# Performance work log

Measured on AMD Instinct MI355X. Metric: run time of the kernel, lower is better.

## Reference

```python
import jax, jax.numpy as jnp
import numpy as np
import math

B, T = 32, 64
VOCAB = 50005
EMB = 512
HID = 1024
SES = 1024
KNOW = 8785
NEG = math.exp(-100)

def _glorot(key, shape):
    fan_in, fan_out = shape[1], shape[0]
    lim = (6.0 / (fan_in + fan_out)) ** 0.5
    return jax.random.uniform(key, shape, jnp.float32, -lim, lim)

def setup_inputs() -> dict:
    key = jax.random.key(0)
    ks = jax.random.split(key, 16)
    inp = {}
    inp['ses_encoding'] = jax.random.normal(ks[0], (B, 1, SES), jnp.float32)
    inp['know_encoding'] = jax.random.normal(ks[1], (B, 1, SES), jnp.float32)
    inp['target'] = jax.random.randint(ks[2], (B, T), 0, 50000)
    inp['embed_w'] = jax.random.normal(ks[3], (VOCAB, EMB), jnp.float32) * 0.02
    # GRU params (PyTorch layout: W_ih [3H, E], W_hh [3H, H], gate order r,z,n)
    s = 1.0 / (HID ** 0.5)
    inp['W_ih'] = jax.random.uniform(ks[4], (3 * HID, EMB), jnp.float32, -s, s)
    inp['W_hh'] = jax.random.uniform(ks[5], (3 * HID, HID), jnp.float32, -s, s)
    inp['b_ih'] = jax.random.uniform(ks[6], (3 * HID,), jnp.float32, -s, s)
    inp['b_hh'] = jax.random.uniform(ks[7], (3 * HID,), jnp.float32, -s, s)
    inp['ses_to_dec_w'] = _glorot(ks[8], (HID, SES))
    inp['ses_to_dec_b'] = jnp.zeros((HID,), jnp.float32)
    inp['dec_inf_w'] = _glorot(ks[9], (2 * EMB, HID))
    inp['ses_inf_w'] = _glorot(ks[10], (2 * EMB, SES))
    inp['emb_inf_w'] = _glorot(ks[11], (2 * EMB, EMB))
    inp['emb_inf_b'] = jnp.zeros((2 * EMB,), jnp.float32)
    inp['W1'] = jax.random.normal(ks[12], (VOCAB, SES), jnp.float32) * 0.02
    inp['W2'] = jax.random.normal(ks[13], (VOCAB, SES), jnp.float32) * 0.02
    inp['W3'] = jax.random.normal(ks[14], (VOCAB, 2 * EMB), jnp.float32) * 0.02
    inp['W4'] = jax.random.normal(ks[15], (VOCAB, EMB), jnp.float32) * 0.02
    inp['know_vote_w'] = _glorot(jax.random.fold_in(key, 99), (KNOW, SES))
    return inp

def _gru_step(x, h, W_ih, W_hh, b_ih, b_hh):
    # x: [B,E], h: [B,H]
    gi = x @ W_ih.T + b_ih
    gh = h @ W_hh.T + b_hh
    ir, iz, inn = jnp.split(gi, 3, axis=-1)
    hr, hz, hn = jnp.split(gh, 3, axis=-1)
    r = jax.nn.sigmoid(ir + hr)
    z = jax.nn.sigmoid(iz + hz)
    n = jnp.tanh(inn + r * hn)
    return (1.0 - z) * h + z * n  # torch: h' = (1-z)*n + z*h with torch z; note torch formula

def _gru_step_torch(x, h, W_ih, W_hh, b_ih, b_hh):
    gi = x @ W_ih.T + b_ih
    gh = h @ W_hh.T + b_hh
    ir, iz, inn = jnp.split(gi, 3, axis=-1)
    hr, hz, hn = jnp.split(gh, 3, axis=-1)
    r = jax.nn.sigmoid(ir + hr)
    z = jax.nn.sigmoid(iz + hz)
    n = jnp.tanh(inn + r * hn)
    return (1.0 - z) * n + z * h

def reference(ses_encoding, know_encoding, target, embed_w, W_ih, W_hh, b_ih, b_hh,
              ses_to_dec_w, ses_to_dec_b, dec_inf_w, ses_inf_w, emb_inf_w, emb_inf_b,
              W1, W2, W3, W4, know_vote_w):
    ses = ses_encoding[:, 0, :]    # [B, SES]
    know = know_encoding[:, 0, :]  # [B, SES]
    target_emb = embed_w[target]   # [B, T, E]

    h0 = jnp.tanh(ses @ ses_to_dec_w.T + ses_to_dec_b)  # [B, H]

    # time-invariant pieces
    ses_inf_vec = ses @ ses_inf_w.T                      # [B, 2E]
    l1 = ses @ W1.T                                      # [B, V]
    l2 = know @ W2.T                                     # [B, V]
    # knowledge mixture log-probs (constant over time)
    ks = know @ know_vote_w.T                            # [B, KNOW]
    ks = ks[:, :-1]                                      # drop last -> [B, KNOW-1]
    pad_l = jnp.full((ks.shape[0], 10), NEG, ks.dtype)
    pad_r = jnp.full((ks.shape[0], VOCAB - 10 - (KNOW - 1)), NEG, ks.dtype)
    know_scores = jnp.concatenate([pad_l, ks, pad_r], axis=1)  # [B, V]
    know_probs = jax.nn.log_softmax(know_scores, axis=-1)      # [B, V]
    gate_const = l1 + l2                                 # [B, V]

    def step(h, emb_t):
        # emb_t: [B, E]
        h_new = _gru_step_torch(emb_t, h, W_ih, W_hh, b_ih, b_hh)  # [B, H]
        dec_hid_vec = h_new @ dec_inf_w.T                          # [B, 2E]
        target_inf = emb_t @ emb_inf_w.T + emb_inf_b               # [B, 2E]
        total = dec_hid_vec + ses_inf_vec + target_inf             # [B, 2E]
        mx = jnp.max(total.reshape(total.shape[0], EMB, 2), axis=-1)  # maxout -> [B, E]
        logits = mx @ embed_w.T                                    # shared embedding -> [B, V]
        hid_probs = jax.nn.log_softmax(logits, axis=-1)
        l3 = h_new @ W3.T                                          # note: W3 applied to hid_o [B,H]... but W3 is [V,2E]
        l4 = emb_t @ W4.T                                          # [B, V]
        gate = jax.nn.sigmoid(gate_const + l3 + l4)                # [B, V]
        final = gate * hid_probs + (1.0 - gate) * know_probs       # [B, V]
        return h_new, final

    # target_emb time-major for scan
    _, outs = jax.lax.scan(step, h0, jnp.swapaxes(target_emb, 0, 1))
    final_scores_all = jnp.swapaxes(outs, 0, 1)  # [B, T, V]
    return final_scores_all
```

## Files before the change

### kernel.cpp

```cpp
#include <hip/hip_runtime.h>

constexpr int VOC  = 50005;
constexpr int VOCP = 50048;
constexpr int VOCP2= 50176;
constexpr int NTM  = 391;
constexpr int NTMP = 400;
constexpr int KSN  = 8784;
constexpr int KSNP = 8832;
constexpr float NPAD = 41221.0f;

typedef unsigned short u16;
typedef __attribute__((ext_vector_type(4))) float f32x4;
typedef __attribute__((ext_vector_type(8))) short bf16x8;

__device__ __forceinline__ float dot4(float4 a, float4 b) {
    return a.x*b.x + a.y*b.y + a.z*b.z + a.w*b.w;
}
__device__ __forceinline__ float sigmoidf_(float x) { return 1.0f / (1.0f + expf(-x)); }
__device__ __forceinline__ u16 f2bf(float f) {
    unsigned x = __float_as_uint(f);
    return (u16)((x + 0x7FFFu + ((x >> 16) & 1u)) >> 16);
}
__device__ __forceinline__ float bf2f(u16 u) { return __uint_as_float(((unsigned)u) << 16); }
template<int AUX>
__device__ __forceinline__ void gload_lds16x(const void* g, void* l) {
    __builtin_amdgcn_global_load_lds((const __attribute__((address_space(1))) unsigned int*)g,
                                     (__attribute__((address_space(3))) unsigned int*)l, 16, 0, AUX);
}
__device__ __forceinline__ void gload_lds16(const void* g, void* l) { gload_lds16x<0>(g, l); }
__device__ __forceinline__ void store_u16_sc(u16* p, u16 v) {
    asm volatile("global_store_short %0, %1, off sc0 sc1" :: "v"(p), "v"((unsigned)v) : "memory");
}

__global__ __launch_bounds__(256) void k_cvt(const float* __restrict__ src, u16* __restrict__ dst,
                                             int ncols, int sld, int dld) {
    int row = blockIdx.x;
    int c = (blockIdx.y * 256 + threadIdx.x) * 4;
    if (c >= ncols) return;
    float4 v = *(const float4*)(src + (size_t)row * sld + c);
    unsigned lo = f2bf(v.x) | ((unsigned)f2bf(v.y) << 16);
    unsigned hi = f2bf(v.z) | ((unsigned)f2bf(v.w) << 16);
    *(uint2*)(dst + (size_t)row * dld + c) = make_uint2(lo, hi);
}

__global__ __launch_bounds__(256) void k_pad0(u16* __restrict__ Aemb, u16* __restrict__ A34,
                                              u16* __restrict__ Awk) {
    int r = VOC + blockIdx.x;
    unsigned* p3 = (unsigned*)(A34 + (size_t)r * 1536);
    for (int i = threadIdx.x; i < 768; i += 256) p3[i] = 0;
    if (r < VOCP) {
        unsigned* pe = (unsigned*)(Aemb + (size_t)r * 512);
        if (threadIdx.x < 256) pe[threadIdx.x] = 0;
        unsigned* pw = (unsigned*)(Awk + (size_t)r * 2048);
        for (int i = threadIdx.x; i < 1024; i += 256) pw[i] = 0;
    }
}
__global__ __launch_bounds__(256) void k_padK(u16* __restrict__ kvwb) {
    int r = KSN + blockIdx.x;
    unsigned* p = (unsigned*)(kvwb + (size_t)r * 1024);
    for (int i = threadIdx.x; i < 512; i += 256) p[i] = 0;
}

__global__ __launch_bounds__(256) void k_bsk(const float* __restrict__ ses,
                                             const float* __restrict__ know,
                                             u16* __restrict__ Bsk) {
    int row = blockIdx.x;
    for (int c0 = threadIdx.x * 4; c0 < 2048; c0 += 1024) {
        uint2 val = make_uint2(0, 0);
        if (row < 32) {
            const float* srcp = (c0 < 1024) ? ses + (size_t)row * 1024 + c0
                                            : know + (size_t)row * 1024 + (c0 - 1024);
            float4 v = *(const float4*)srcp;
            val = make_uint2(f2bf(v.x) | ((unsigned)f2bf(v.y) << 16),
                             f2bf(v.z) | ((unsigned)f2bf(v.w) << 16));
        }
        *(uint2*)(Bsk + (size_t)row * 2048 + c0) = val;
    }
}

__global__ __launch_bounds__(128) void k_gather(const float* __restrict__ embed,
                                                const int* __restrict__ target,
                                                u16* __restrict__ BG) {
    int n = blockIdx.x;
    int row = target[n];
    int c = threadIdx.x * 4;
    float4 v = *(const float4*)(embed + (size_t)row * 512 + c);
    unsigned lo = f2bf(v.x) | ((unsigned)f2bf(v.y) << 16);
    unsigned hi = f2bf(v.z) | ((unsigned)f2bf(v.w) << 16);
    *(uint2*)(BG + (size_t)n * 1536 + 1024 + c) = make_uint2(lo, hi);
}

__global__ __launch_bounds__(256) void k_h0_sesinf(const float* __restrict__ ses,
                                                   const float* __restrict__ sdw,
                                                   const float* __restrict__ sdb,
                                                   const float* __restrict__ siw,
                                                   float* __restrict__ h0,
                                                   float* __restrict__ sesinf) {
    int g = blockIdx.x * 256 + threadIdx.x;
    int b = g & 31;
    int jg = g >> 5;
    int j0 = jg * 4;
    const float4* s4 = (const float4*)(ses + (size_t)b * 1024);
    const float4* wa[4];
    const float4* wc[4];
#pragma unroll
    for (int r = 0; r < 4; ++r) {
        wa[r] = (const float4*)(sdw + (size_t)(j0 + r) * 1024);
        wc[r] = (const float4*)(siw + (size_t)(j0 + r) * 1024);
    }
    float a[4] = {0, 0, 0, 0}, c[4] = {0, 0, 0, 0};
    for (int kq = 0; kq < 256; ++kq) {
        float4 sv = s4[kq];
#pragma unroll
        for (int r = 0; r < 4; ++r) { a[r] += dot4(sv, wa[r][kq]); c[r] += dot4(sv, wc[r][kq]); }
    }
#pragma unroll
    for (int r = 0; r < 4; ++r) {
        h0[b * 1024 + j0 + r] = tanhf(a[r] + sdb[j0 + r]);
        sesinf[b * 1024 + j0 + r] = c[r];
    }
}

__global__ __launch_bounds__(256) void k_lseknow(const float* __restrict__ ks,
                                                 float* __restrict__ lsek) {
    int b = blockIdx.x;
    int t = threadIdx.x;
    __shared__ float sm[256];
    float m = -1e30f;
    for (int j = t; j < KSN; j += 256) m = fmaxf(m, ks[(size_t)b * KSN + j]);
    sm[t] = m;
    __syncthreads();
    for (int s = 128; s > 0; s >>= 1) { if (t < s) sm[t] = fmaxf(sm[t], sm[t + s]); __syncthreads(); }
    m = fmaxf(sm[0], 0.0f);
    __syncthreads();
    float s = 0.0f;
    for (int j = t; j < KSN; j += 256) s += expf(ks[(size_t)b * KSN + j] - m);
    sm[t] = s;
    __syncthreads();
    for (int r = 128; r > 0; r >>= 1) { if (t < r) sm[t] += sm[t + r]; __syncthreads(); }
    if (t == 0) lsek[b] = m + logf(sm[0] + NPAD * expf(0.0f - m));
}

template<int EPI>
__global__ __launch_bounds__(256) void gemm_bt(
    const u16* __restrict__ A, int lda,
    const u16* __restrict__ B, int ldb, int K,
    const float* __restrict__ p0, const float* __restrict__ p1,
    float* __restrict__ q0, u16* __restrict__ q1,
    unsigned char* __restrict__ q2, float* __restrict__ q3)
{
    __shared__ u16 Asm[128 * 64];
    __shared__ u16 Bsm[128 * 64];
    const int tid = threadIdx.x;
    const int lane = tid & 63;
    const int w = tid >> 6;
    const int wm = w >> 1, wn = w & 1;
    const int nt = blockIdx.x, mt = blockIdx.y;

    f32x4 acc[4][4];
#pragma unroll
    for (int i = 0; i < 4; ++i)
#pragma unroll
        for (int j = 0; j < 4; ++j) acc[i][j] = (f32x4){0.f, 0.f, 0.f, 0.f};

    for (int kt = 0; kt < K; kt += 64) {
#pragma unroll
        for (int p = 0; p < 4; ++p) {
            int flat = (w * 4 + p) * 64 + lane;
            int row = flat >> 3, slot = flat & 7;
            int ss = slot ^ (row & 7);
            gload_lds16(A + (size_t)(mt * 128 + row) * lda + kt + ss * 8, Asm + flat * 8);
            gload_lds16(B + (size_t)(nt * 128 + row) * ldb + kt + ss * 8, Bsm + flat * 8);
        }
        __syncthreads();
#pragma unroll
        for (int kc = 0; kc < 2; ++kc) {
            bf16x8 af[4], bfr[4];
#pragma unroll
            for (int mi = 0; mi < 4; ++mi) {
                int row = wm * 64 + mi * 16 + (lane & 15);
                int bcol = kc * 64 + ((lane >> 4) << 4);
                af[mi] = *(const bf16x8*)((const char*)Asm + row * 128 + (bcol ^ ((row & 7) << 4)));
            }
#pragma unroll
            for (int ni = 0; ni < 4; ++ni) {
                int row = wn * 64 + ni * 16 + (lane & 15);
                int bcol = kc * 64 + ((lane >> 4) << 4);
                bfr[ni] = *(const bf16x8*)((const char*)Bsm + row * 128 + (bcol ^ ((row & 7) << 4)));
            }
#pragma unroll
            for (int mi = 0; mi < 4; ++mi)
#pragma unroll
                for (int ni = 0; ni < 4; ++ni)
                    acc[mi][ni] = __builtin_amdgcn_mfma_f32_16x16x32_bf16(af[mi], bfr[ni], acc[mi][ni], 0, 0, 0);
        }
        __syncthreads();
    }

    const int cl = lane & 15;
    const int rg = (lane >> 4) << 2;

    if constexpr (EPI == 0) {
#pragma unroll
        for (int mi = 0; mi < 4; ++mi) {
            int m0 = mt * 128 + wm * 64 + mi * 16 + rg;
            float4 bias = *(const float4*)(p0 + m0);
#pragma unroll
            for (int ni = 0; ni < 4; ++ni) {
                int n = nt * 128 + wn * 64 + ni * 16 + cl;
                float4 v;
                v.x = acc[mi][ni][0] + bias.x; v.y = acc[mi][ni][1] + bias.y;
                v.z = acc[mi][ni][2] + bias.z; v.w = acc[mi][ni][3] + bias.w;
                *(float4*)(q0 + (size_t)n * 3072 + m0) = v;
            }
        }
    }
    if constexpr (EPI == 1) {
#pragma unroll
        for (int mi = 0; mi < 4; ++mi) {
            int m0 = mt * 128 + wm * 64 + mi * 16 + rg;
            float4 eb4 = *(const float4*)(p1 + m0);
#pragma unroll
            for (int ni = 0; ni < 4; ++ni) {
                int n = nt * 128 + wn * 64 + ni * 16 + cl;
                int b = n >> 6;
                float v0 = acc[mi][ni][0] + p0[b * 1024 + m0 + 0] + eb4.x;
                float v1 = acc[mi][ni][1] + p0[b * 1024 + m0 + 1] + eb4.y;
                float v2 = acc[mi][ni][2] + p0[b * 1024 + m0 + 2] + eb4.z;
                float v3 = acc[mi][ni][3] + p0[b * 1024 + m0 + 3] + eb4.w;
                unsigned pk = f2bf(fmaxf(v0, v1)) | ((unsigned)f2bf(fmaxf(v2, v3)) << 16);
                *(unsigned*)(q1 + (size_t)n * 512 + (m0 >> 1)) = pk;
            }
        }
    }
    if constexpr (EPI == 3) {
        __shared__ float redm[2][128];
        __shared__ float reds[2][128];
#pragma unroll
        for (int mi = 0; mi < 4; ++mi) {
            int v0 = mt * 128 + wm * 64 + mi * 16 + rg;
#pragma unroll
            for (int ni = 0; ni < 4; ++ni) {
                int n = nt * 128 + wn * 64 + ni * 16 + cl;
                unsigned lo = f2bf(acc[mi][ni][0]) | ((unsigned)f2bf(acc[mi][ni][1]) << 16);
                unsigned hi = f2bf(acc[mi][ni][2]) | ((unsigned)f2bf(acc[mi][ni][3]) << 16);
                *(uint2*)(q1 + (size_t)n * VOCP + v0) = make_uint2(lo, hi);
            }
        }
#pragma unroll
        for (int ni = 0; ni < 4; ++ni) {
            float lm = -1e30f;
#pragma unroll
            for (int mi = 0; mi < 4; ++mi) {
                int v0 = mt * 128 + wm * 64 + mi * 16 + rg;
#pragma unroll
                for (int r = 0; r < 4; ++r)
                    if (v0 + r < VOC) lm = fmaxf(lm, acc[mi][ni][r]);
            }
            lm = fmaxf(lm, __shfl_xor(lm, 16));
            lm = fmaxf(lm, __shfl_xor(lm, 32));
            float s = 0.0f;
#pragma unroll
            for (int mi = 0; mi < 4; ++mi) {
                int v0 = mt * 128 + wm * 64 + mi * 16 + rg;
#pragma unroll
                for (int r = 0; r < 4; ++r)
                    if (v0 + r < VOC) s += expf(acc[mi][ni][r] - lm);
            }
            s += __shfl_xor(s, 16);
            s += __shfl_xor(s, 32);
            if (lane < 16) {
                redm[wm][wn * 64 + ni * 16 + lane] = lm;
                reds[wm][wn * 64 + ni * 16 + lane] = s;
            }
        }
        __syncthreads();
        if (tid < 128) {
            float m0_ = redm[0][tid], m1_ = redm[1][tid];
            float m = fmaxf(m0_, m1_);
            float s = reds[0][tid] * expf(m0_ - m) + reds[1][tid] * expf(m1_ - m);
            int n = nt * 128 + tid;
            q0[(size_t)n * NTMP + mt] = m;
            q3[(size_t)n * NTMP + mt] = s;
        }
    }
    if constexpr (EPI == 4) {
#pragma unroll
        for (int mi = 0; mi < 4; ++mi) {
            int m0 = mt * 128 + wm * 64 + mi * 16 + rg;
#pragma unroll
            for (int ni = 0; ni < 4; ++ni) {
                int n = nt * 128 + wn * 64 + ni * 16 + cl;
                if (n < 32) {
                    float4 v;
                    v.x = acc[mi][ni][0]; v.y = acc[mi][ni][1];
                    v.z = acc[mi][ni][2]; v.w = acc[mi][ni][3];
                    *(float4*)(q0 + (size_t)n * VOCP2 + m0) = v;
                }
            }
        }
    }
    if constexpr (EPI == 5) {
#pragma unroll
        for (int mi = 0; mi < 4; ++mi) {
            int m0 = mt * 128 + wm * 64 + mi * 16 + rg;
#pragma unroll
            for (int ni = 0; ni < 4; ++ni) {
                int n = nt * 128 + wn * 64 + ni * 16 + cl;
                if (n < 32 && m0 < KSN) {
                    float4 v;
                    v.x = acc[mi][ni][0]; v.y = acc[mi][ni][1];
                    v.z = acc[mi][ni][2]; v.w = acc[mi][ni][3];
                    *(float4*)(q0 + (size_t)n * KSN + m0) = v;
                }
            }
        }
    }
}

__global__ __launch_bounds__(512, 1) void gemm_gate8(
    const u16* __restrict__ A,
    const u16* __restrict__ B,
    const float* __restrict__ gc2,
    unsigned char* __restrict__ g8)
{
    __shared__ __align__(16) char smem[131072];
    const int tid = threadIdx.x;
    const int lane = tid & 63;
    const int w = tid >> 6;
    const int wm = w >> 2;
    const int wn = w & 3;
    const int lrow = lane & 15;
    const int g = lane >> 4;

    int bid = blockIdx.x;
    int wg = (bid & 7) * 196 + (bid >> 3);
    int mt = wg >> 3;
    int nt = wg & 7;
    const size_t arow0 = (size_t)mt * 256;
    const size_t brow0 = (size_t)nt * 256;

    auto stageA = [&](int T, int h) {
        char* dst = smem + (T & 1) * 65536 + h * 16384;
        const u16* src = A + (arow0 + h * 128) * 1536 + T * 64;
#pragma unroll
        for (int q = 0; q < 2; ++q) {
            int flat = q * 512 + tid;
            int r = flat >> 3, s = flat & 7;
            int ss = s ^ (r & 7);
            gload_lds16(src + (size_t)r * 1536 + ss * 8, dst + flat * 16);
        }
    };
    auto stageB = [&](int T, int h) {
        char* dst = smem + (T & 1) * 65536 + 32768 + h * 16384;
        const u16* src = B + (brow0 + h * 128) * 1536 + T * 64;
#pragma unroll
        for (int q = 0; q < 2; ++q) {
            int flat = q * 512 + tid;
            int r = flat >> 3, s = flat & 7;
            int ss = s ^ (r & 7);
            gload_lds16(src + (size_t)r * 1536 + ss * 8, dst + flat * 16);
        }
    };

    f32x4 acc[8][4];
#pragma unroll
    for (int i = 0; i < 8; ++i)
#pragma unroll
        for (int j = 0; j < 4; ++j) acc[i][j] = (f32x4){0.f, 0.f, 0.f, 0.f};

    bf16x8 bf[4][2];
    auto loadB_ = [&](int d) {
        char* Bb = smem + d * 65536 + 32768 + (wn >> 1) * 16384;
#pragma unroll
        for (int ni = 0; ni < 4; ++ni) {
            int r = (wn & 1) * 64 + ni * 16 + lrow;
#pragma unroll
            for (int kk = 0; kk < 2; ++kk)
                bf[ni][kk] = *(const bf16x8*)(Bb + r * 128 + ((kk * 64 + g * 16) ^ ((r & 7) << 4)));
        }
    };

#define GPH(D, Q, LB, STG, VM)                                                        \
    {                                                                                 \
        if (LB) loadB_(D);                                                            \
        bf16x8 af[2][2];                                                              \
        char* Ab = smem + (D) * 65536 + wm * 16384;                                   \
        _Pragma("unroll") for (int mi = 0; mi < 2; ++mi) {                            \
            int r = ((Q) * 2 + mi) * 16 + lrow;                                       \
            _Pragma("unroll") for (int kk = 0; kk < 2; ++kk)                          \
                af[mi][kk] = *(const bf16x8*)(Ab + r * 128 +                          \
                                ((kk * 64 + g * 16) ^ ((r & 7) << 4)));               \
        }                                                                             \
        STG;                                                                          \
        __builtin_amdgcn_s_barrier();                                                 \
        asm volatile("s_waitcnt lgkmcnt(0)" ::: "memory");                            \
        __builtin_amdgcn_sched_barrier(0);                                            \
        __builtin_amdgcn_s_setprio(1);                                                \
        _Pragma("unroll") for (int kk = 0; kk < 2; ++kk)                              \
            _Pragma("unroll") for (int mi = 0; mi < 2; ++mi)                          \
                _Pragma("unroll") for (int ni = 0; ni < 4; ++ni)                      \
                    acc[(Q) * 2 + mi][ni] = __builtin_amdgcn_mfma_f32_16x16x32_bf16(  \
                        af[mi][kk], bf[ni][kk], acc[(Q) * 2 + mi][ni], 0, 0, 0);      \
        __builtin_amdgcn_s_setprio(0);                                                \
        VM;                                                                           \
        __builtin_amdgcn_s_barrier();                                                 \
    }
#define VM4 asm volatile("s_waitcnt vmcnt(4)" ::: "memory"); __builtin_amdgcn_sched_barrier(0)
#define VM0 asm volatile("s_waitcnt vmcnt(0)" ::: "memory"); __builtin_amdgcn_sched_barrier(0)
#define NOP (void)0

    stageB(0, 0); stageB(0, 1); stageA(0, 0); stageA(0, 1); stageB(1, 0); stageB(1, 1);
    VM4;
    __builtin_amdgcn_s_barrier();

    for (int i = 0; i < 11; ++i) {
        int T0 = 2 * i, T1 = 2 * i + 1;
        GPH(0, 0, true,  stageA(T1, 0),     NOP);
        GPH(0, 1, false, stageA(T1, 1),     NOP);
        GPH(0, 2, false, stageB(T0 + 2, 0), NOP);
        GPH(0, 3, false, stageB(T0 + 2, 1), VM4);
        GPH(1, 0, true,  stageA(T0 + 2, 0), NOP);
        GPH(1, 1, false, stageA(T0 + 2, 1), NOP);
        GPH(1, 2, false, stageB(T1 + 2, 0), NOP);
        GPH(1, 3, false, stageB(T1 + 2, 1), VM4);
    }
    GPH(0, 0, true,  stageA(23, 0), NOP);
    GPH(0, 1, false, stageA(23, 1), NOP);
    GPH(0, 2, false, NOP,           NOP);
    GPH(0, 3, false, NOP,           VM0);
    GPH(1, 0, true,  NOP,           NOP);
    GPH(1, 1, false, NOP,           NOP);
    GPH(1, 2, false, NOP,           NOP);
    GPH(1, 3, false, NOP,           NOP);
#undef GPH
#undef VM4
#undef VM0
#undef NOP

    const int rg = g << 2;
    const int b = nt * 4 + wn;
    const float* gcrow = gc2 + (size_t)b * VOCP2;
#pragma unroll
    for (int m = 0; m < 8; ++m) {
        int v0 = mt * 256 + wm * 128 + m * 16 + rg;
        float4 gcv = *(const float4*)(gcrow + v0);
#pragma unroll
        for (int ni = 0; ni < 4; ++ni) {
            int n = nt * 256 + wn * 64 + ni * 16 + lrow;
            unsigned pk = 0;
#pragma unroll
            for (int r = 0; r < 4; ++r) {
                float garg = acc[m][ni][r] + ((const float*)&gcv)[r];
                float gate = 1.0f / (1.0f + expf(-garg));
                pk |= ((unsigned)(int)(gate * 255.0f + 0.5f)) << (8 * r);
            }
            *(unsigned*)(g8 + (size_t)n * VOCP2 + v0) = pk;
        }
    }
}

__global__ __launch_bounds__(256, 1) void k_gru_m4(const u16* __restrict__ WhhB,
                                                   const float* __restrict__ GI,
                                                   const float* __restrict__ bhh,
                                                   const u16* __restrict__ h0b,
                                                   u16* __restrict__ BG,
                                                   unsigned* __restrict__ flags) {
    __shared__ __align__(16) char smem[131072];
    const int tid = threadIdx.x;
    const int lane = tid & 63;
    const int w = tid >> 6;
    const int jb = blockIdx.x;
    const int j0 = jb * 16;
    const int jl = tid & 15, bp = tid >> 4;
    const int je = j0 + jl;
    const float bh0 = bhh[je], bh1 = bhh[1024 + je], bh2 = bhh[2048 + je];
    char* Bbase = smem + 98304 + w * 8192;

#pragma unroll
    for (int it = 0; it < 24; ++it) {
        int flat = (it * 4 + w) * 64 + lane;
        int r = flat >> 7, s = flat & 127;
        int ss = s ^ (r & 7);
        int gr = (r >> 4) * 1024 + j0 + (r & 15);
        gload_lds16(WhhB + (size_t)gr * 1024 + ss * 8, smem + (size_t)flat * 16);
    }

    float hpv[2];
#pragma unroll
    for (int rb = 0; rb < 2; ++rb)
        hpv[rb] = bf2f(h0b[(size_t)(bp * 2 + rb) * 1024 + je]);

    const int lrow = lane & 15;
    const int ksel = lane >> 4;

    for (int t = 0; t < 64; ++t) {
        const u16* hsrc = (t == 0) ? h0b : BG + (size_t)(t - 1) * 1536;
        const size_t hstr = (t == 0) ? 1024 : (size_t)64 * 1536;

        float gi0[2], gi1[2], gi2[2];
#pragma unroll
        for (int rb = 0; rb < 2; ++rb) {
            const float* gp = GI + ((size_t)((bp * 2 + rb) * 64 + t)) * 3072 + je;
            gi0[rb] = gp[0]; gi1[rb] = gp[1024]; gi2[rb] = gp[2048];
        }
        __builtin_amdgcn_sched_barrier(0);

        auto stageB = [&](int c) {
            char* dst = Bbase + (c & 1) * 4096;
            int kq0 = w * 256 + c * 64;
#pragma unroll
            for (int q = 0; q < 4; ++q) {
                int flat = q * 64 + lane;
                int r = flat >> 3, s = flat & 7;
                int ss = s ^ (r & 7);
                gload_lds16x<0x11>(hsrc + (size_t)r * hstr + kq0 + ss * 8,
                                   dst + (size_t)flat * 16);
            }
        };
        stageB(0); stageB(1);
        if (t == 0) {
            __syncthreads();
        } else {
            asm volatile("s_waitcnt vmcnt(4)" ::: "memory");
        }
        __builtin_amdgcn_sched_barrier(0);

        f32x4 acc[3][2];
#pragma unroll
        for (int mi = 0; mi < 3; ++mi)
#pragma unroll
            for (int ni = 0; ni < 2; ++ni) acc[mi][ni] = (f32x4){0.f, 0.f, 0.f, 0.f};

#pragma unroll
        for (int c = 0; c < 4; ++c) {
            char* Bb = Bbase + (c & 1) * 4096;
#pragma unroll
            for (int ks = 0; ks < 2; ++ks) {
                int kb = ks * 64 + ksel * 16;
                bf16x8 bfr[2];
#pragma unroll
                for (int ni = 0; ni < 2; ++ni) {
                    int br = ni * 16 + lrow;
                    bfr[ni] = *(const bf16x8*)(Bb + br * 128 + (kb ^ ((br & 7) << 4)));
                }
                int kA = w * 512 + c * 128 + kb;
#pragma unroll
                for (int mi = 0; mi < 3; ++mi) {
                    int ar = mi * 16 + lrow;
                    bf16x8 af = *(const bf16x8*)(smem + ar * 2048 + (kA ^ ((ar & 7) << 4)));
#pragma unroll
                    for (int ni = 0; ni < 2; ++ni)
                        acc[mi][ni] = __builtin_amdgcn_mfma_f32_16x16x32_bf16(af, bfr[ni], acc[mi][ni], 0, 0, 0);
                }
            }
            asm volatile("s_waitcnt lgkmcnt(0)" ::: "memory");
            __builtin_amdgcn_sched_barrier(0);
            if (c < 2) {
                stageB(c + 2);
                asm volatile("s_waitcnt vmcnt(4)" ::: "memory");
            } else if (c == 2) {
                asm volatile("s_waitcnt vmcnt(0)" ::: "memory");
            }
            __builtin_amdgcn_sched_barrier(0);
        }

        float (*epiw)[33] = (float(*)[33])Bbase;
        {
            const int rg = (lane >> 4) << 2;
#pragma unroll
            for (int mi = 0; mi < 3; ++mi)
#pragma unroll
                for (int ni = 0; ni < 2; ++ni) {
                    int m0 = mi * 16 + rg;
                    int cb = ni * 16 + lrow;
#pragma unroll
                    for (int r = 0; r < 4; ++r) epiw[m0 + r][cb] = acc[mi][ni][r];
                }
        }
        asm volatile("s_waitcnt lgkmcnt(0)" ::: "memory");
        __builtin_amdgcn_s_barrier();

#pragma unroll
        for (int rb = 0; rb < 2; ++rb) {
            int b = bp * 2 + rb;
            float s0 = 0.f, s1 = 0.f, s2 = 0.f;
#pragma unroll
            for (int ww = 0; ww < 4; ++ww) {
                float (*ep)[33] = (float(*)[33])(smem + 98304 + ww * 8192);
                s0 += ep[jl][b]; s1 += ep[16 + jl][b]; s2 += ep[32 + jl][b];
            }
            float rr = sigmoidf_(gi0[rb] + s0 + bh0);
            float zz = sigmoidf_(gi1[rb] + s1 + bh1);
            float nn = tanhf(gi2[rb] + rr * (s2 + bh2));
            float hnew = (1.0f - zz) * nn + zz * hpv[rb];
            hpv[rb] = hnew;
            store_u16_sc(BG + ((size_t)(b * 64 + t)) * 1536 + je, f2bf(hnew));
        }

        if (t < 63) {
            asm volatile("s_waitcnt vmcnt(0)" ::: "memory");
            __syncthreads();
            if (tid == 0)
                __hip_atomic_store(&flags[jb], (unsigned)(t + 1),
                                   __ATOMIC_RELAXED, __HIP_MEMORY_SCOPE_AGENT);
            unsigned tgt = (unsigned)(t + 1);
            while (true) {
                unsigned v = __hip_atomic_load(&flags[lane],
                                               __ATOMIC_RELAXED, __HIP_MEMORY_SCOPE_AGENT);
                if (__all(v >= tgt)) break;
                __builtin_amdgcn_s_sleep(1);
            }
            __builtin_amdgcn_sched_barrier(0);
        }
    }
}

__global__ __launch_bounds__(256) void k_lse(const float* __restrict__ pmax,
                                             const float* __restrict__ psum,
                                             float* __restrict__ lse) {
    int n = blockIdx.x;
    int t = threadIdx.x;
    __shared__ float sm[256];
    const float* pm = pmax + (size_t)n * NTMP;
    const float* ps = psum + (size_t)n * NTMP;
    float m = -1e30f;
    for (int p = t; p < NTM; p += 256) m = fmaxf(m, pm[p]);
    sm[t] = m;
    __syncthreads();
    for (int s = 128; s > 0; s >>= 1) { if (t < s) sm[t] = fmaxf(sm[t], sm[t + s]); __syncthreads(); }
    m = sm[0];
    __syncthreads();
    float s = 0.0f;
    for (int p = t; p < NTM; p += 256) s += ps[p] * expf(pm[p] - m);
    sm[t] = s;
    __syncthreads();
    for (int r = 128; r > 0; r >>= 1) { if (t < r) sm[t] += sm[t + r]; __syncthreads(); }
    if (t == 0) lse[n] = m + logf(sm[0]);
}

__global__ __launch_bounds__(256) void k_final(const u16* __restrict__ Lb,
                                               const unsigned char* __restrict__ g8,
                                               const float* __restrict__ lse,
                                               const float* __restrict__ ks,
                                               const float* __restrict__ lsek,
                                               float* __restrict__ out) {
    int n = blockIdx.y;
    int b = n >> 6;
    float lsen = lse[n], lkb = lsek[b];
    int base = blockIdx.x * 2048;
#pragma unroll
    for (int i = 0; i < 8; ++i) {
        int v = base + i * 256 + threadIdx.x;
        if (v < VOC) {
            float L = bf2f(Lb[(size_t)n * VOCP + v]);
            float g = g8[(size_t)n * VOCP2 + v] * (1.0f / 255.0f);
            float kp = ((v >= 10 && v < 10 + KSN) ? ks[(size_t)b * KSN + (v - 10)] : 0.0f) - lkb;
            out[(size_t)n * VOC + v] = g * (L - lsen) + (1.0f - g) * kp;
        }
    }
}

extern "C" void kernel_launch(void* const* d_in, const int* in_sizes, int n_in,
                              void* d_out, int out_size, void* d_ws, size_t ws_size,
                              hipStream_t stream) {
    const float* ses    = (const float*)d_in[0];
    const float* know   = (const float*)d_in[1];
    const int*   target = (const int*)d_in[2];
    const float* embed  = (const float*)d_in[3];
    const float* Wih    = (const float*)d_in[4];
    const float* Whh    = (const float*)d_in[5];
    const float* bih    = (const float*)d_in[6];
    const float* bhh    = (const float*)d_in[7];
    const float* sdw    = (const float*)d_in[8];
    const float* sdb    = (const float*)d_in[9];
    const float* dw     = (const float*)d_in[10];
    const float* siw    = (const float*)d_in[11];
    const float* ew     = (const float*)d_in[12];
    const float* eb     = (const float*)d_in[13];
    const float* W1     = (const float*)d_in[14];
    const float* W2     = (const float*)d_in[15];
    const float* W3     = (const float*)d_in[16];
    const float* W4     = (const float*)d_in[17];
    const float* kvw    = (const float*)d_in[18];

    char* ws = (char*)d_ws;
    size_t o = 0;
    auto alloc = [&](size_t bytes) { char* r = ws + o; o += (bytes + 255) & ~(size_t)255; return r; };
    u16*   Aemb  = (u16*)  alloc((size_t)VOCP * 512 * 2);
    u16*   A34   = (u16*)  alloc((size_t)VOCP2 * 1536 * 2);
    u16*   Adwew = (u16*)  alloc((size_t)1024 * 1536 * 2);
    u16*   Wihb  = (u16*)  alloc((size_t)3072 * 512 * 2);
    u16*   WhhB  = (u16*)  alloc((size_t)3072 * 1024 * 2);
    u16*   h0b   = (u16*)  alloc((size_t)32 * 1024 * 2);
    u16*   BG    = (u16*)  alloc((size_t)2048 * 1536 * 2);
    u16*   BL    = (u16*)  alloc((size_t)2048 * 512 * 2);
    float* GI    = (float*)alloc((size_t)2048 * 3072 * 4);
    float* h0    = (float*)alloc((size_t)32 * 1024 * 4);
    float* sesinf= (float*)alloc((size_t)32 * 1024 * 4);
    float* gc    = (float*)alloc((size_t)32 * VOCP2 * 4);
    float* ksb   = (float*)alloc((size_t)32 * KSN * 4);
    float* lsek  = (float*)alloc(256);
    float* lse   = (float*)alloc((size_t)2048 * 4);
    unsigned* flags = (unsigned*)alloc(256);
    float* pmax  = (float*)alloc((size_t)2048 * NTMP * 4);
    float* psum  = (float*)alloc((size_t)2048 * NTMP * 4);
    unsigned char* g8 = (unsigned char*)alloc((size_t)2048 * VOCP2);
    u16*   Lb    = (u16*)  alloc((size_t)2048 * VOCP * 2);
    u16*   Bsk   = (u16*)  alloc((size_t)128 * 2048 * 2);
    float* out = (float*)d_out;

    u16*   kvwb  = (u16*)g8;
    u16*   Awk   = Lb;

    hipMemsetAsync(flags, 0, 256, stream);

    k_cvt<<<dim3(VOC, 1), 256, 0, stream>>>(embed, Aemb, 512, 512, 512);
    k_cvt<<<dim3(VOC, 1), 256, 0, stream>>>(W3, A34, 1024, 1024, 1536);
    k_cvt<<<dim3(VOC, 1), 256, 0, stream>>>(W4, A34 + 1024, 512, 512, 1536);
    k_cvt<<<dim3(VOC, 1), 256, 0, stream>>>(W1, Awk, 1024, 1024, 2048);
    k_cvt<<<dim3(VOC, 1), 256, 0, stream>>>(W2, Awk + 1024, 1024, 1024, 2048);
    k_cvt<<<dim3(KSN, 1), 256, 0, stream>>>(kvw, kvwb, 1024, 1024, 1024);
    k_pad0<<<dim3(VOCP2 - VOC), 256, 0, stream>>>(Aemb, A34, Awk);
    k_padK<<<dim3(KSNP - KSN), 256, 0, stream>>>(kvwb);
    k_cvt<<<dim3(1024, 1), 256, 0, stream>>>(dw, Adwew, 1024, 1024, 1536);
    k_cvt<<<dim3(1024, 1), 256, 0, stream>>>(ew, Adwew + 1024, 512, 512, 1536);
    k_cvt<<<dim3(3072, 1), 256, 0, stream>>>(Wih, Wihb, 512, 512, 512);
    k_cvt<<<dim3(3072, 1), 256, 0, stream>>>(Whh, WhhB, 1024, 1024, 1024);
    k_bsk<<<dim3(128), 256, 0, stream>>>(ses, know, Bsk);

    k_gather<<<dim3(2048), 128, 0, stream>>>(embed, target, BG);
    k_h0_sesinf<<<dim3(32), 256, 0, stream>>>(ses, sdw, sdb, siw, h0, sesinf);
    k_cvt<<<dim3(32, 1), 256, 0, stream>>>(h0, h0b, 1024, 1024, 1024);

    gemm_bt<4><<<dim3(1, NTM), 256, 0, stream>>>(Awk, 2048, Bsk, 2048, 2048,
                                                 nullptr, nullptr, gc, nullptr, nullptr, nullptr);
    gemm_bt<5><<<dim3(1, 69), 256, 0, stream>>>(kvwb, 1024, Bsk + 1024, 2048, 1024,
                                                nullptr, nullptr, ksb, nullptr, nullptr, nullptr);
    k_lseknow<<<dim3(32), 256, 0, stream>>>(ksb, lsek);

    gemm_bt<0><<<dim3(16, 24), 256, 0, stream>>>(Wihb, 512, BG + 1024, 1536, 512,
                                                 bih, nullptr, GI, nullptr, nullptr, nullptr);
    k_gru_m4<<<dim3(64), 256, 0, stream>>>(WhhB, GI, bhh, h0b, BG, flags);
    gemm_bt<1><<<dim3(16, 8), 256, 0, stream>>>(Adwew, 1536, BG, 1536, 1536,
                                                sesinf, eb, nullptr, BL, nullptr, nullptr);
    gemm_gate8<<<dim3(1568), 512, 0, stream>>>(A34, BG, gc, g8);
    gemm_bt<3><<<dim3(16, NTM), 256, 0, stream>>>(Aemb, 512, BL, 512, 512,
                                                  nullptr, nullptr, pmax, Lb, nullptr, psum);
    k_lse<<<dim3(2048), 256, 0, stream>>>(pmax, psum, lse);
    k_final<<<dim3(25, 2048), 256, 0, stream>>>(Lb, g8, lse, ksb, lsek, out);
}
```

Measured before the change: 1.634 ms.

## Fuse fp32-to-bf16 conversion into skinny W1/W2/know GEMMs and regroup gate8 barriers

Replaces the separate bf16 conversion passes over W1, W2 and know_vote_w, plus their padded gemm_bt launches, with a dedicated skinny-N MFMA kernel. That kernel reads the fp32 weights directly, packs them to bf16 in registers and multiplies them against the 32-column Bsk matrix. This removes a full write and re-read of large bf16 copies of those weights, along with the padding kernels. Separately, the gate8 GEMM pipeline moves staging to the start of each phase and issues barriers every two phases instead of twice per phase, aiming to cut synchronization stalls. The trade-off is that the new kernel has no LDS reuse and uses small 128-thread blocks, and the barrier regrouping could expose LDS hazards if staging and reads overlap incorrectly.

Result: faster. 1.569 ms (-4.0%).

```diff
diff --git a/kernel.cpp b/kernel.cpp
--- a/kernel.cpp
+++ b/kernel.cpp
@@ -6,7 +6,6 @@
 constexpr int NTM  = 391;
 constexpr int NTMP = 400;
 constexpr int KSN  = 8784;
-constexpr int KSNP = 8832;
 constexpr float NPAD = 41221.0f;
 
 typedef unsigned short u16;
@@ -22,6 +21,14 @@
     return (u16)((x + 0x7FFFu + ((x >> 16) & 1u)) >> 16);
 }
 __device__ __forceinline__ float bf2f(u16 u) { return __uint_as_float(((unsigned)u) << 16); }
+__device__ __forceinline__ bf16x8 pack8(float4 lo, float4 hi) {
+    union { bf16x8 v; unsigned u[4]; } r;
+    r.u[0] = f2bf(lo.x) | ((unsigned)f2bf(lo.y) << 16);
+    r.u[1] = f2bf(lo.z) | ((unsigned)f2bf(lo.w) << 16);
+    r.u[2] = f2bf(hi.x) | ((unsigned)f2bf(hi.y) << 16);
+    r.u[3] = f2bf(hi.z) | ((unsigned)f2bf(hi.w) << 16);
+    return r.v;
+}
 template<int AUX>
 __device__ __forceinline__ void gload_lds16x(const void* g, void* l) {
     __builtin_amdgcn_global_load_lds((const __attribute__((address_space(1))) unsigned int*)g,
@@ -43,22 +50,14 @@
     *(uint2*)(dst + (size_t)row * dld + c) = make_uint2(lo, hi);
 }
 
-__global__ __launch_bounds__(256) void k_pad0(u16* __restrict__ Aemb, u16* __restrict__ A34,
-                                              u16* __restrict__ Awk) {
+__global__ __launch_bounds__(256) void k_pad0(u16* __restrict__ Aemb, u16* __restrict__ A34) {
     int r = VOC + blockIdx.x;
     unsigned* p3 = (unsigned*)(A34 + (size_t)r * 1536);
     for (int i = threadIdx.x; i < 768; i += 256) p3[i] = 0;
     if (r < VOCP) {
         unsigned* pe = (unsigned*)(Aemb + (size_t)r * 512);
         if (threadIdx.x < 256) pe[threadIdx.x] = 0;
-        unsigned* pw = (unsigned*)(Awk + (size_t)r * 2048);
-        for (int i = threadIdx.x; i < 1024; i += 256) pw[i] = 0;
-    }
-}
-__global__ __launch_bounds__(256) void k_padK(u16* __restrict__ kvwb) {
-    int r = KSN + blockIdx.x;
-    unsigned* p = (unsigned*)(kvwb + (size_t)r * 1024);
-    for (int i = threadIdx.x; i < 512; i += 256) p[i] = 0;
+    }
 }
 
 __global__ __launch_bounds__(256) void k_bsk(const float* __restrict__ ses,
@@ -141,6 +140,57 @@
     if (t == 0) lsek[b] = m + logf(sm[0] + NPAD * expf(0.0f - m));
 }
 
+template<int MODE>
+__global__ __launch_bounds__(128) void k_sk32(const float* __restrict__ A1,
+                                              const float* __restrict__ A2,
+                                              const u16* __restrict__ Bsk,
+                                              float* __restrict__ outp) {
+    const int lane = threadIdx.x & 63;
+    const int w = threadIdx.x >> 6;
+    const int lrow = lane & 15;
+    const int kg = lane >> 4;
+    constexpr int K = (MODE == 0) ? 2048 : 1024;
+    constexpr int bc0 = (MODE == 0) ? 0 : 1024;
+    const int rowmax = (MODE == 0) ? (VOC - 1) : (KSN - 1);
+    const int vb = blockIdx.x * 64 + w * 32;
+    const int r0 = min(vb + lrow, rowmax);
+    const int r1 = min(vb + 16 + lrow, rowmax);
+    f32x4 acc[2][2] = {{{0.f,0.f,0.f,0.f},{0.f,0.f,0.f,0.f}},
+                       {{0.f,0.f,0.f,0.f},{0.f,0.f,0.f,0.f}}};
+    for (int k0 = 0; k0 < K; k0 += 32) {
+        int kc = k0 + kg * 8;
+        const float* s0;
+        const float* s1;
+        if (MODE == 0 && k0 >= 1024) {
+            s0 = A2 + (size_t)r0 * 1024 + (kc - 1024);
+            s1 = A2 + (size_t)r1 * 1024 + (kc - 1024);
+        } else {
+            s0 = A1 + (size_t)r0 * 1024 + kc;
+            s1 = A1 + (size_t)r1 * 1024 + kc;
+        }
+        bf16x8 af0 = pack8(*(const float4*)s0, *(const float4*)(s0 + 4));
+        bf16x8 af1 = pack8(*(const float4*)s1, *(const float4*)(s1 + 4));
+        bf16x8 b0 = *(const bf16x8*)(Bsk + (size_t)lrow * 2048 + bc0 + kc);
+        bf16x8 b1 = *(const bf16x8*)(Bsk + (size_t)(16 + lrow) * 2048 + bc0 + kc);
+        acc[0][0] = __builtin_amdgcn_mfma_f32_16x16x32_bf16(af0, b0, acc[0][0], 0, 0, 0);
+        acc[0][1] = __builtin_amdgcn_mfma_f32_16x16x32_bf16(af0, b1, acc[0][1], 0, 0, 0);
+        acc[1][0] = __builtin_amdgcn_mfma_f32_16x16x32_bf16(af1, b0, acc[1][0], 0, 0, 0);
+        acc[1][1] = __builtin_amdgcn_mfma_f32_16x16x32_bf16(af1, b1, acc[1][1], 0, 0, 0);
+    }
+    const int rg = kg * 4;
+#pragma unroll
+    for (int mi = 0; mi < 2; ++mi)
+#pragma unroll
+        for (int ni = 0; ni < 2; ++ni)
+#pragma unroll
+            for (int r = 0; r < 4; ++r) {
+                int v = vb + mi * 16 + rg + r;
+                int b = ni * 16 + lrow;
+                if (MODE == 0) outp[(size_t)b * VOCP2 + v] = acc[mi][ni][r];
+                else if (v < KSN) outp[(size_t)b * KSN + v] = acc[mi][ni][r];
+            }
+}
+
 template<int EPI>
 __global__ __launch_bounds__(256) void gemm_bt(
     const u16* __restrict__ A, int lda,
@@ -284,38 +334,6 @@
             q3[(size_t)n * NTMP + mt] = s;
         }
     }
-    if constexpr (EPI == 4) {
-#pragma unroll
-        for (int mi = 0; mi < 4; ++mi) {
-            int m0 = mt * 128 + wm * 64 + mi * 16 + rg;
-#pragma unroll
-            for (int ni = 0; ni < 4; ++ni) {
-                int n = nt * 128 + wn * 64 + ni * 16 + cl;
-                if (n < 32) {
-                    float4 v;
-                    v.x = acc[mi][ni][0]; v.y = acc[mi][ni][1];
-                    v.z = acc[mi][ni][2]; v.w = acc[mi][ni][3];
-                    *(float4*)(q0 + (size_t)n * VOCP2 + m0) = v;
-                }
-            }
-        }
-    }
-    if constexpr (EPI == 5) {
-#pragma unroll
-        for (int mi = 0; mi < 4; ++mi) {
-            int m0 = mt * 128 + wm * 64 + mi * 16 + rg;
-#pragma unroll
-            for (int ni = 0; ni < 4; ++ni) {
-                int n = nt * 128 + wn * 64 + ni * 16 + cl;
-                if (n < 32 && m0 < KSN) {
-                    float4 v;
-                    v.x = acc[mi][ni][0]; v.y = acc[mi][ni][1];
-                    v.z = acc[mi][ni][2]; v.w = acc[mi][ni][3];
-                    *(float4*)(q0 + (size_t)n * KSN + m0) = v;
-                }
-            }
-        }
-    }
 }
 
 __global__ __launch_bounds__(512, 1) void gemm_gate8(
@@ -381,8 +399,9 @@
         }
     };
 
-#define GPH(D, Q, LB, STG, VM)                                                        \
+#define GPH2(D, Q, LB, STG)                                                           \
     {                                                                                 \
+        STG;                                                                          \
         if (LB) loadB_(D);                                                            \
         bf16x8 af[2][2];                                                              \
         char* Ab = smem + (D) * 65536 + wm * 16384;                                   \
@@ -392,8 +411,6 @@
                 af[mi][kk] = *(const bf16x8*)(Ab + r * 128 +                          \
                                 ((kk * 64 + g * 16) ^ ((r & 7) << 4)));               \
         }                                                                             \
-        STG;                                                                          \
-        __builtin_amdgcn_s_barrier();                                                 \
         asm volatile("s_waitcnt lgkmcnt(0)" ::: "memory");                            \
         __builtin_amdgcn_sched_barrier(0);                                            \
         __builtin_amdgcn_s_setprio(1);                                                \
@@ -403,40 +420,47 @@
                     acc[(Q) * 2 + mi][ni] = __builtin_amdgcn_mfma_f32_16x16x32_bf16(  \
                         af[mi][kk], bf[ni][kk], acc[(Q) * 2 + mi][ni], 0, 0, 0);      \
         __builtin_amdgcn_s_setprio(0);                                                \
-        VM;                                                                           \
-        __builtin_amdgcn_s_barrier();                                                 \
-    }
+    }
+#define BARR  __builtin_amdgcn_sched_barrier(0); __builtin_amdgcn_s_barrier(); \
+              __builtin_amdgcn_sched_barrier(0)
 #define VM4 asm volatile("s_waitcnt vmcnt(4)" ::: "memory"); __builtin_amdgcn_sched_barrier(0)
 #define VM0 asm volatile("s_waitcnt vmcnt(0)" ::: "memory"); __builtin_amdgcn_sched_barrier(0)
-#define NOP (void)0
+#define NOPX (void)0
 
     stageB(0, 0); stageB(0, 1); stageA(0, 0); stageA(0, 1); stageB(1, 0); stageB(1, 1);
     VM4;
-    __builtin_amdgcn_s_barrier();
+    BARR;
 
     for (int i = 0; i < 11; ++i) {
         int T0 = 2 * i, T1 = 2 * i + 1;
-        GPH(0, 0, true,  stageA(T1, 0),     NOP);
-        GPH(0, 1, false, stageA(T1, 1),     NOP);
-        GPH(0, 2, false, stageB(T0 + 2, 0), NOP);
-        GPH(0, 3, false, stageB(T0 + 2, 1), VM4);
-        GPH(1, 0, true,  stageA(T0 + 2, 0), NOP);
-        GPH(1, 1, false, stageA(T0 + 2, 1), NOP);
-        GPH(1, 2, false, stageB(T1 + 2, 0), NOP);
-        GPH(1, 3, false, stageB(T1 + 2, 1), VM4);
-    }
-    GPH(0, 0, true,  stageA(23, 0), NOP);
-    GPH(0, 1, false, stageA(23, 1), NOP);
-    GPH(0, 2, false, NOP,           NOP);
-    GPH(0, 3, false, NOP,           VM0);
-    GPH(1, 0, true,  NOP,           NOP);
-    GPH(1, 1, false, NOP,           NOP);
-    GPH(1, 2, false, NOP,           NOP);
-    GPH(1, 3, false, NOP,           NOP);
-#undef GPH
+        GPH2(0, 0, true,  stageA(T1, 0));
+        GPH2(0, 1, false, stageA(T1, 1));
+        BARR;
+        GPH2(0, 2, false, stageB(T0 + 2, 0));
+        GPH2(0, 3, false, stageB(T0 + 2, 1));
+        VM4; BARR;
+        GPH2(1, 0, true,  stageA(T0 + 2, 0));
+        GPH2(1, 1, false, stageA(T0 + 2, 1));
+        BARR;
+        GPH2(1, 2, false, stageB(T1 + 2, 0));
+        GPH2(1, 3, false, stageB(T1 + 2, 1));
+        VM4; BARR;
+    }
+    GPH2(0, 0, true,  stageA(23, 0));
+    GPH2(0, 1, false, stageA(23, 1));
+    BARR;
+    GPH2(0, 2, false, NOPX);
+    GPH2(0, 3, false, NOPX);
+    VM0; BARR;
+    GPH2(1, 0, true,  NOPX);
+    GPH2(1, 1, false, NOPX);
+    GPH2(1, 2, false, NOPX);
+    GPH2(1, 3, false, NOPX);
+#undef GPH2
+#undef BARR
 #undef VM4
 #undef VM0
-#undef NOP
+#undef NOPX
 
     const int rg = g << 2;
     const int b = nt * 4 + wn;
@@ -710,19 +734,12 @@
     u16*   Bsk   = (u16*)  alloc((size_t)128 * 2048 * 2);
     float* out = (float*)d_out;
 
-    u16*   kvwb  = (u16*)g8;
-    u16*   Awk   = Lb;
-
     hipMemsetAsync(flags, 0, 256, stream);
 
     k_cvt<<<dim3(VOC, 1), 256, 0, stream>>>(embed, Aemb, 512, 512, 512);
     k_cvt<<<dim3(VOC, 1), 256, 0, stream>>>(W3, A34, 1024, 1024, 1536);
     k_cvt<<<dim3(VOC, 1), 256, 0, stream>>>(W4, A34 + 1024, 512, 512, 1536);
-    k_cvt<<<dim3(VOC, 1), 256, 0, stream>>>(W1, Awk, 1024, 1024, 2048);
-    k_cvt<<<dim3(VOC, 1), 256, 0, stream>>>(W2, Awk + 1024, 1024, 1024, 2048);
-    k_cvt<<<dim3(KSN, 1), 256, 0, stream>>>(kvw, kvwb, 1024, 1024, 1024);
-    k_pad0<<<dim3(VOCP2 - VOC), 256, 0, stream>>>(Aemb, A34, Awk);
-    k_padK<<<dim3(KSNP - KSN), 256, 0, stream>>>(kvwb);
+    k_pad0<<<dim3(VOCP2 - VOC), 256, 0, stream>>>(Aemb, A34);
     k_cvt<<<dim3(1024, 1), 256, 0, stream>>>(dw, Adwew, 1024, 1024, 1536);
     k_cvt<<<dim3(1024, 1), 256, 0, stream>>>(ew, Adwew + 1024, 512, 512, 1536);
     k_cvt<<<dim3(3072, 1), 256, 0, stream>>>(Wih, Wihb, 512, 512, 512);
@@ -733,10 +750,8 @@
     k_h0_sesinf<<<dim3(32), 256, 0, stream>>>(ses, sdw, sdb, siw, h0, sesinf);
     k_cvt<<<dim3(32, 1), 256, 0, stream>>>(h0, h0b, 1024, 1024, 1024);
 
-    gemm_bt<4><<<dim3(1, NTM), 256, 0, stream>>>(Awk, 2048, Bsk, 2048, 2048,
-                                                 nullptr, nullptr, gc, nullptr, nullptr, nullptr);
-    gemm_bt<5><<<dim3(1, 69), 256, 0, stream>>>(kvwb, 1024, Bsk + 1024, 2048, 1024,
-                                                nullptr, nullptr, ksb, nullptr, nullptr, nullptr);
+    k_sk32<0><<<dim3(VOCP2 / 64), 128, 0, stream>>>(W1, W2, Bsk, gc);
+    k_sk32<1><<<dim3((KSN + 63) / 64), 128, 0, stream>>>(kvw, nullptr, Bsk, ksb);
     k_lseknow<<<dim3(32), 256, 0, stream>>>(ksb, lsek);
 
     gemm_bt<0><<<dim3(16, 24), 256, 0, stream>>>(Wihb, 512, BG + 1024, 1536, 512,
```
